# Kernel optimization log

Measured on AMD Instinct MI355X. Metric: run time of the kernel, lower is better.

## Reference

```python
import jax, jax.numpy as jnp
import numpy as np

N = 4096
NFEAT = 512
NHID = 64
NHEADS = 8
NCLASS = 41
ALPHA = 0.2          # LeakyReLU negative slope
NEG = -9e15          # mask fill value from the torch code
EDGE_P = 0.004       # ~16 avg degree


def _xavier_uniform(key, shape, gain=1.414):
    fan_in, fan_out = shape[-2], shape[-1]
    limit = gain * np.sqrt(6.0 / (fan_in + fan_out))
    return jax.random.uniform(key, shape, jnp.float32, -limit, limit)


def setup_inputs() -> dict:
    key = jax.random.key(0)
    ks = jax.random.split(key, 6)
    x = jax.random.normal(ks[0], (N, NFEAT), jnp.float32)
    # sparse random graph, densified (module calls adj.to_dense()); add self-loops
    adj = (jax.random.uniform(ks[1], (N, N)) < EDGE_P).astype(jnp.float32)
    adj = jnp.maximum(adj, jnp.eye(N, dtype=jnp.float32))
    # 8 attention heads (nfeat -> nhid), stacked
    W_heads = _xavier_uniform(ks[2], (NHEADS, NFEAT, NHID))
    a_heads = _xavier_uniform(ks[3], (NHEADS, 2 * NHID, 1))
    # output attention layer (nhid*nheads -> nclass)
    W_out = _xavier_uniform(ks[4], (NHEADS * NHID, NCLASS))
    a_out = _xavier_uniform(ks[5], (2 * NCLASS, 1))
    return {"x": x, "adj": adj, "W_heads": W_heads, "a_heads": a_heads,
            "W_out": W_out, "a_out": a_out}


def _leaky_relu(e):
    return jnp.where(e > 0, e, ALPHA * e)


def reference(x, adj, W_heads, a_heads, W_out, a_out):
    # inference mode: all dropout layers are identity (training=False)
    mask = adj > 0                                   # [N, N]
    # ---- multi-head GAT layer (concat=True, ELU inside layer) ----
    Wh = jnp.einsum('nf,hfd->hnd', x, W_heads)       # [H, N, D]
    a1 = a_heads[:, :NHID, 0]                        # [H, D]
    a2 = a_heads[:, NHID:, 0]                        # [H, D]
    s1 = jnp.einsum('hnd,hd->hn', Wh, a1)            # [H, N]
    s2 = jnp.einsum('hnd,hd->hn', Wh, a2)            # [H, N]
    e = _leaky_relu(s1[:, :, None] + s2[:, None, :])  # [H, N, N]
    att = jax.nn.softmax(jnp.where(mask[None], e, NEG), axis=-1)
    h = jax.nn.elu(jnp.einsum('hnm,hmd->hnd', att, Wh))   # [H, N, D]
    h = jnp.transpose(h, (1, 0, 2)).reshape(N, NHEADS * NHID)  # concat heads
    # ---- output GAT layer (concat=False) + ELU (with_relu=True) ----
    Wh2 = h @ W_out                                  # [N, C]
    e2 = _leaky_relu(Wh2 @ a_out[:NCLASS] + (Wh2 @ a_out[NCLASS:]).T)  # [N, N]
    att2 = jax.nn.softmax(jnp.where(mask, e2, NEG), axis=-1)
    out = jax.nn.elu(att2 @ Wh2)                     # [N, C]
    # mode='t', multi_label falsy -> log_softmax
    return jax.nn.log_softmax(out, axis=1)
```

## Files before the change

### kernel.cpp

```cpp
#include <hip/hip_runtime.h>
#include <hip/hip_bf16.h>
#include <math.h>


#define N 4096
#define NFEAT 512
#define NHID 64
#define NHEADS 8
#define NCLASS 41
#define NCPAD 48
#define ALPHA 0.2f
#define ELLW 64

using short8  = __attribute__((ext_vector_type(8))) short;
using floatx4 = __attribute__((ext_vector_type(4))) float;

__device__ __forceinline__ float wred_max(float v) {
#pragma unroll
  for (int o = 32; o; o >>= 1) v = fmaxf(v, __shfl_xor(v, o, 64));
  return v;
}
__device__ __forceinline__ float wred_sum(float v) {
#pragma unroll
  for (int o = 32; o; o >>= 1) v += __shfl_xor(v, o, 64);
  return v;
}

__device__ __forceinline__ void split_bf16(float v, short& hi, short& lo) {
  __hip_bfloat16 hb = __float2bfloat16(v);
  float hf = __bfloat162float(hb);
  __hip_bfloat16 lb = __float2bfloat16(v - hf);
  hi = *reinterpret_cast<short*>(&hb);
  lo = *reinterpret_cast<short*>(&lb);
}

__global__ __launch_bounds__(256) void setup(const float* __restrict__ x,
                                             const float* __restrict__ W,
                                             const float* __restrict__ W_out,
                                             const float* __restrict__ adj,
                                             short* __restrict__ Xhi,
                                             short* __restrict__ Xlo,
                                             short* __restrict__ Wthi,
                                             short* __restrict__ Wtlo,
                                             short* __restrict__ WOhi,
                                             short* __restrict__ WOlo,
                                             int* __restrict__ cols,
                                             int* __restrict__ cnts) {
  if (blockIdx.x < 4096) {
    __shared__ int c;
    const int row = blockIdx.x;
    if (threadIdx.x == 0) c = 0;
    __syncthreads();
    const float4* arow = (const float4*)(adj + (size_t)row * N);
    for (int j4 = threadIdx.x; j4 < N / 4; j4 += 256) {
      float4 v = arow[j4];
      if (v.x > 0.f) { int p = atomicAdd(&c, 1); if (p < ELLW) cols[row * ELLW + p] = j4 * 4 + 0; }
      if (v.y > 0.f) { int p = atomicAdd(&c, 1); if (p < ELLW) cols[row * ELLW + p] = j4 * 4 + 1; }
      if (v.z > 0.f) { int p = atomicAdd(&c, 1); if (p < ELLW) cols[row * ELLW + p] = j4 * 4 + 2; }
      if (v.w > 0.f) { int p = atomicAdd(&c, 1); if (p < ELLW) cols[row * ELLW + p] = j4 * 4 + 3; }
    }
    __syncthreads();
    if (threadIdx.x == 0) cnts[row] = min(c, ELLW);
  } else if (blockIdx.x < 6144) {
    const int t = (blockIdx.x - 4096) * 256 + threadIdx.x;
    const float4 v = ((const float4*)x)[t];
    short h0, l0, h1, l1, h2, l2, h3, l3;
    split_bf16(v.x, h0, l0);
    split_bf16(v.y, h1, l1);
    split_bf16(v.z, h2, l2);
    split_bf16(v.w, h3, l3);
    ((short4*)Xhi)[t] = make_short4(h0, h1, h2, h3);
    ((short4*)Xlo)[t] = make_short4(l0, l1, l2, l3);
  } else if (blockIdx.x < 6208) {
    __shared__ float tile[64][65];
    const int idx = blockIdx.x - 6144;
    const int h = idx >> 3, k0 = (idx & 7) * 64;
    const int t = threadIdx.x;
#pragma unroll
    for (int i = 0; i < 4; i++) {
      const int g = t + 256 * i;
      const int r = g >> 4, c4 = g & 15;
      const float4 v = *(const float4*)&W[(size_t)h * 32768 + (size_t)(k0 + r) * 64 + c4 * 4];
      tile[r][c4 * 4 + 0] = v.x;
      tile[r][c4 * 4 + 1] = v.y;
      tile[r][c4 * 4 + 2] = v.z;
      tile[r][c4 * 4 + 3] = v.w;
    }
    __syncthreads();
#pragma unroll
    for (int i = 0; i < 2; i++) {
      const int g = t + 256 * i;
      const int d = g >> 3, kg = (g & 7) * 8;
      short8 hv, lv;
#pragma unroll
      for (int j = 0; j < 8; j++) {
        short hh, ll;
        split_bf16(tile[kg + j][d], hh, ll);
        hv[j] = hh;
        lv[j] = ll;
      }
      const size_t dst = (size_t)h * 32768 + (size_t)d * 512 + k0 + kg;
      *(short8*)&Wthi[dst] = hv;
      *(short8*)&Wtlo[dst] = lv;
    }
  } else {
    const int t = (blockIdx.x - 6208) * 256 + threadIdx.x;
    const int c = t >> 9, k = t & 511;
    float v = (c < NCLASS) ? W_out[(size_t)k * NCLASS + c] : 0.f;
    short hi, lo;
    split_bf16(v, hi, lo);
    WOhi[c * 512 + k] = hi;
    WOlo[c * 512 + k] = lo;
  }
}

__global__ __launch_bounds__(128) void wh_gemm_mfma(
    const short* __restrict__ Xhi, const short* __restrict__ Xlo,
    const short* __restrict__ Wthi, const short* __restrict__ Wtlo,
    const float* __restrict__ a_heads,
    float* __restrict__ Wh, float* __restrict__ s1, float* __restrict__ s2) {
  __shared__ __align__(16) short Ahi[64 * 72];
  __shared__ __align__(16) short Alo[64 * 72];
  __shared__ __align__(16) short Bhi[64 * 72];
  __shared__ __align__(16) short Blo[64 * 72];
  const int id = blockIdx.x;
  const int h = (id >> 3) & 7;
  const int tile = (id & 7) + ((id >> 6) << 3);
  const int n0 = tile * 64;
  const int tid = threadIdx.x;
  const int w = tid >> 6, L = tid & 63;

  floatx4 acc[2][4];
#pragma unroll
  for (int rt = 0; rt < 2; rt++)
#pragma unroll
    for (int f = 0; f < 4; f++) acc[rt][f] = (floatx4){0.f, 0.f, 0.f, 0.f};

  for (int k0 = 0; k0 < NFEAT; k0 += 64) {
    __syncthreads();
#pragma unroll
    for (int i = 0; i < 4; i++) {
      const int g = tid + 128 * i;
      const int row = g >> 3, kg = (g & 7) * 8;
      const size_t asrc = (size_t)(n0 + row) * NFEAT + k0 + kg;
      *(uint4*)&Ahi[row * 72 + kg] = *(const uint4*)&Xhi[asrc];
      *(uint4*)&Alo[row * 72 + kg] = *(const uint4*)&Xlo[asrc];
      const size_t bsrc = (size_t)h * 32768 + (size_t)row * 512 + k0 + kg;
      *(uint4*)&Bhi[row * 72 + kg] = *(const uint4*)&Wthi[bsrc];
      *(uint4*)&Blo[row * 72 + kg] = *(const uint4*)&Wtlo[bsrc];
    }
    __syncthreads();
#pragma unroll
    for (int ks = 0; ks < 2; ks++) {
      const int koff = ks * 32 + (L >> 4) * 8;
      const int abase = (w * 32 + (L & 15)) * 72 + koff;
      short8 ahi0 = *(const short8*)&Ahi[abase];
      short8 alo0 = *(const short8*)&Alo[abase];
      short8 ahi1 = *(const short8*)&Ahi[abase + 16 * 72];
      short8 alo1 = *(const short8*)&Alo[abase + 16 * 72];
#pragma unroll
      for (int f = 0; f < 4; f++) {
        short8 bhi = *(const short8*)&Bhi[(f * 16 + (L & 15)) * 72 + koff];
        short8 blo = *(const short8*)&Blo[(f * 16 + (L & 15)) * 72 + koff];
        acc[0][f] = __builtin_amdgcn_mfma_f32_16x16x32_bf16(ahi0, bhi, acc[0][f], 0, 0, 0);
        acc[0][f] = __builtin_amdgcn_mfma_f32_16x16x32_bf16(ahi0, blo, acc[0][f], 0, 0, 0);
        acc[0][f] = __builtin_amdgcn_mfma_f32_16x16x32_bf16(alo0, bhi, acc[0][f], 0, 0, 0);
        acc[1][f] = __builtin_amdgcn_mfma_f32_16x16x32_bf16(ahi1, bhi, acc[1][f], 0, 0, 0);
        acc[1][f] = __builtin_amdgcn_mfma_f32_16x16x32_bf16(ahi1, blo, acc[1][f], 0, 0, 0);
        acc[1][f] = __builtin_amdgcn_mfma_f32_16x16x32_bf16(alo1, bhi, acc[1][f], 0, 0, 0);
      }
    }
  }

  const int q = L >> 4, c16 = L & 15;
  float a1v[4], a2v[4];
#pragma unroll
  for (int f = 0; f < 4; f++) {
    a1v[f] = a_heads[h * 128 + f * 16 + c16];
    a2v[f] = a_heads[h * 128 + 64 + f * 16 + c16];
  }
#pragma unroll
  for (int rt = 0; rt < 2; rt++) {
    float p1[4] = {0.f, 0.f, 0.f, 0.f}, p2[4] = {0.f, 0.f, 0.f, 0.f};
#pragma unroll
    for (int f = 0; f < 4; f++)
#pragma unroll
      for (int r = 0; r < 4; r++) {
        const float vv = acc[rt][f][r];
        const int row = n0 + w * 32 + rt * 16 + q * 4 + r;
        Wh[((size_t)(h << 12) + row) * NHID + f * 16 + c16] = vv;
        p1[r] += vv * a1v[f];
        p2[r] += vv * a2v[f];
      }
#pragma unroll
    for (int r = 0; r < 4; r++)
#pragma unroll
      for (int o = 1; o < 16; o <<= 1) {
        p1[r] += __shfl_xor(p1[r], o, 64);
        p2[r] += __shfl_xor(p2[r], o, 64);
      }
    if (c16 == 0) {
      const int row = n0 + w * 32 + rt * 16 + q * 4;
#pragma unroll
      for (int r = 0; r < 4; r++) {
        s1[(h << 12) + row + r] = p1[r];
        s2[(h << 12) + row + r] = p2[r];
      }
    }
  }
}

__global__ __launch_bounds__(256) void att1_kernel(
    const float* __restrict__ Wh, const float* __restrict__ s1,
    const float* __restrict__ s2, const int* __restrict__ cols,
    const int* __restrict__ cnts, short* __restrict__ Hhi,
    short* __restrict__ Hlo) {
  __shared__ float pj[4][64];
  __shared__ int jj[4][64];
  const int w = threadIdx.x >> 6, lane = threadIdx.x & 63;
  const int pair = blockIdx.x * 4 + w;
  const int h = pair >> 12, i = pair & (N - 1);
  const int cnt = cnts[i];
  const float s1i = s1[(h << 12) + i];
  const float* s2h = s2 + (h << 12);
  float e0 = -1e30f;
  int j0 = 0;
  if (lane < cnt) {
    j0 = cols[i * ELLW + lane];
    float t = s1i + s2h[j0];
    e0 = t > 0.f ? t : ALPHA * t;
  }
  const float m = wred_max(e0);
  float p = (lane < cnt) ? expf(e0 - m) : 0.f;
  const float S = wred_sum(p);
  p *= 1.f / S;
  pj[w][lane] = p;
  jj[w][lane] = (lane < cnt) ? j0 : 0;
  __syncthreads();
  const int grp = lane >> 3, c8 = lane & 7;
  const float* Whh = Wh + (((size_t)h << 12)) * NHID;
  float4 a0 = make_float4(0.f, 0.f, 0.f, 0.f);
  float4 a1 = make_float4(0.f, 0.f, 0.f, 0.f);
  for (int t0 = 0; t0 < cnt; t0 += 8) {
    const float pt = pj[w][t0 + grp];
    const int jt = jj[w][t0 + grp];
    const float4 v0 = *(const float4*)&Whh[(size_t)jt * NHID + c8 * 8];
    const float4 v1 = *(const float4*)&Whh[(size_t)jt * NHID + c8 * 8 + 4];
    a0.x += pt * v0.x; a0.y += pt * v0.y; a0.z += pt * v0.z; a0.w += pt * v0.w;
    a1.x += pt * v1.x; a1.y += pt * v1.y; a1.z += pt * v1.z; a1.w += pt * v1.w;
  }
#pragma unroll
  for (int off = 8; off <= 32; off <<= 1) {
    a0.x += __shfl_xor(a0.x, off, 64);
    a0.y += __shfl_xor(a0.y, off, 64);
    a0.z += __shfl_xor(a0.z, off, 64);
    a0.w += __shfl_xor(a0.w, off, 64);
    a1.x += __shfl_xor(a1.x, off, 64);
    a1.y += __shfl_xor(a1.y, off, 64);
    a1.z += __shfl_xor(a1.z, off, 64);
    a1.w += __shfl_xor(a1.w, off, 64);
  }
  if (grp == 0) {
    float o[8] = {a0.x, a0.y, a0.z, a0.w, a1.x, a1.y, a1.z, a1.w};
    short8 hv, lv;
#pragma unroll
    for (int j = 0; j < 8; j++) {
      const float e = o[j] > 0.f ? o[j] : expf(o[j]) - 1.f;
      short hh, ll;
      split_bf16(e, hh, ll);
      hv[j] = hh;
      lv[j] = ll;
    }
    const size_t base = (size_t)i * 512 + h * 64 + c8 * 8;
    *(short8*)&Hhi[base] = hv;
    *(short8*)&Hlo[base] = lv;
  }
}

__global__ __launch_bounds__(256) void gemm2_mfma(
    const short* __restrict__ Hhi, const short* __restrict__ Hlo,
    const short* __restrict__ WOhi, const short* __restrict__ WOlo,
    const float* __restrict__ a_out,
    float* __restrict__ Wh2, float* __restrict__ s1b, float* __restrict__ s2b) {
  __shared__ float red[3][64][12];
  const int n0 = blockIdx.x * 16;
  const int tid = threadIdx.x;
  const int w = tid >> 6, L = tid & 63;
  const int r15 = L & 15;

  floatx4 acc[3];
#pragma unroll
  for (int f = 0; f < 3; f++) acc[f] = (floatx4){0.f, 0.f, 0.f, 0.f};

#pragma unroll
  for (int ks = 0; ks < 4; ks++) {
    const int koff = w * 128 + ks * 32 + (L >> 4) * 8;
    const short8 ahi = *(const short8*)&Hhi[(size_t)(n0 + r15) * 512 + koff];
    const short8 alo = *(const short8*)&Hlo[(size_t)(n0 + r15) * 512 + koff];
#pragma unroll
    for (int f = 0; f < 3; f++) {
      const short8 bhi = *(const short8*)&WOhi[(size_t)(f * 16 + r15) * 512 + koff];
      const short8 blo = *(const short8*)&WOlo[(size_t)(f * 16 + r15) * 512 + koff];
      acc[f] = __builtin_amdgcn_mfma_f32_16x16x32_bf16(ahi, bhi, acc[f], 0, 0, 0);
      acc[f] = __builtin_amdgcn_mfma_f32_16x16x32_bf16(ahi, blo, acc[f], 0, 0, 0);
      acc[f] = __builtin_amdgcn_mfma_f32_16x16x32_bf16(alo, bhi, acc[f], 0, 0, 0);
    }
  }

  if (w) {
#pragma unroll
    for (int f = 0; f < 3; f++)
#pragma unroll
      for (int r = 0; r < 4; r++) red[w - 1][L][f * 4 + r] = acc[f][r];
  }
  __syncthreads();
  if (w == 0) {
    const int q = L >> 4, c16 = r15;
    float a1v[3], a2v[3];
#pragma unroll
    for (int f = 0; f < 3; f++) {
      const int col = f * 16 + c16;
      a1v[f] = (col < NCLASS) ? a_out[col] : 0.f;
      a2v[f] = (col < NCLASS) ? a_out[NCLASS + col] : 0.f;
    }
    float p1[4] = {0.f, 0.f, 0.f, 0.f}, p2[4] = {0.f, 0.f, 0.f, 0.f};
#pragma unroll
    for (int f = 0; f < 3; f++)
#pragma unroll
      for (int r = 0; r < 4; r++) {
        const float vv = acc[f][r] + red[0][L][f * 4 + r] + red[1][L][f * 4 + r] +
                         red[2][L][f * 4 + r];
        const int col = f * 16 + c16;
        const int row = n0 + q * 4 + r;
        if (col < NCLASS) Wh2[(size_t)row * NCLASS + col] = vv;
        p1[r] += vv * a1v[f];
        p2[r] += vv * a2v[f];
      }
#pragma unroll
    for (int r = 0; r < 4; r++)
#pragma unroll
      for (int o = 1; o < 16; o <<= 1) {
        p1[r] += __shfl_xor(p1[r], o, 64);
        p2[r] += __shfl_xor(p2[r], o, 64);
      }
    if (c16 == 0) {
      const int row = n0 + q * 4;
#pragma unroll
      for (int r = 0; r < 4; r++) {
        s1b[row + r] = p1[r];
        s2b[row + r] = p2[r];
      }
    }
  }
}

__global__ __launch_bounds__(256) void att2_kernel(const float* __restrict__ Wh2,
                                                   const float* __restrict__ s1b,
                                                   const float* __restrict__ s2b,
                                                   const int* __restrict__ cols,
                                                   const int* __restrict__ cnts,
                                                   float* __restrict__ out) {
  __shared__ float pj[4][64];
  __shared__ int jj[4][64];
  const int w = threadIdx.x >> 6, lane = threadIdx.x & 63;
  const int i = blockIdx.x * 4 + w;
  const int cnt = cnts[i];
  const float s1i = s1b[i];
  float e0 = -1e30f;
  int j0 = 0;
  if (lane < cnt) {
    j0 = cols[i * ELLW + lane];
    float t = s1i + s2b[j0];
    e0 = t > 0.f ? t : ALPHA * t;
  }
  const float m = wred_max(e0);
  float p = (lane < cnt) ? expf(e0 - m) : 0.f;
  const float S = wred_sum(p);
  p *= 1.f / S;
  pj[w][lane] = p;
  jj[w][lane] = (lane < cnt) ? j0 : 0;
  __syncthreads();
  float acc = 0.f;
  for (int t = 0; t < cnt; t++) {
    const float pt = pj[w][t];
    const int jt = jj[w][t];
    if (lane < NCLASS) acc += pt * Wh2[(size_t)jt * NCLASS + lane];
  }
  const float o = acc > 0.f ? acc : expf(acc) - 1.f;
  const float vv = (lane < NCLASS) ? o : -1e30f;
  const float mm = wred_max(vv);
  const float ex = (lane < NCLASS) ? expf(o - mm) : 0.f;
  const float SS = wred_sum(ex);
  if (lane < NCLASS) out[(size_t)i * NCLASS + lane] = o - mm - logf(SS);
}

extern "C" void kernel_launch(void* const* d_in, const int* in_sizes, int n_in,
                              void* d_out, int out_size, void* d_ws, size_t ws_size,
                              hipStream_t stream) {
  const float* x       = (const float*)d_in[0];
  const float* adj     = (const float*)d_in[1];
  const float* W_heads = (const float*)d_in[2];
  const float* a_heads = (const float*)d_in[3];
  const float* W_out   = (const float*)d_in[4];
  const float* a_out   = (const float*)d_in[5];
  float* out = (float*)d_out;

  float* ws   = (float*)d_ws;
  float* Wh   = ws;
  float* s1   = Wh + (size_t)NHEADS * N * NHID;
  float* s2   = s1 + NHEADS * N;
  float* Wh2  = s2 + NHEADS * N;
  float* s1b  = Wh2 + (size_t)N * NCLASS;
  float* s2b  = s1b + N;
  int* cnts   = (int*)(s2b + N);
  int* cols   = cnts + N;
  short* Xhi  = (short*)(cols + N * ELLW);
  short* Xlo  = Xhi + (size_t)N * NFEAT;
  short* Wthi = Xlo + (size_t)N * NFEAT;
  short* Wtlo = Wthi + (size_t)NHEADS * NHID * NFEAT;
  short* WOhi = Wtlo + (size_t)NHEADS * NHID * NFEAT;
  short* WOlo = WOhi + (size_t)NCPAD * 512;
  short* Hhi  = WOlo + (size_t)NCPAD * 512;
  short* Hlo  = Hhi + (size_t)N * NFEAT;

  hipLaunchKernelGGL(setup, dim3(6304), dim3(256), 0, stream,
                     x, W_heads, W_out, adj, Xhi, Xlo, Wthi, Wtlo, WOhi, WOlo, cols, cnts);
  hipLaunchKernelGGL(wh_gemm_mfma, dim3(NHEADS * N / 64), dim3(128), 0, stream,
                     Xhi, Xlo, Wthi, Wtlo, a_heads, Wh, s1, s2);
  hipLaunchKernelGGL(att1_kernel, dim3(NHEADS * N / 4), dim3(256), 0, stream,
                     Wh, s1, s2, cols, cnts, Hhi, Hlo);
  hipLaunchKernelGGL(gemm2_mfma, dim3(N / 16), dim3(256), 0, stream,
                     Hhi, Hlo, WOhi, WOlo, a_out, Wh2, s1b, s2b);
  hipLaunchKernelGGL(att2_kernel, dim3(N / 4), dim3(256), 0, stream,
                     Wh2, s1b, s2b, cols, cnts, out);
}
```

Before: 160.1 us.

## Drop LDS staging in Wh GEMM, load MFMA operands directly from global

Rewrites the per-head Wh GEMM so each wave loads its bf16 hi/lo A and B fragments straight from global memory instead of staging 64x64 tiles in shared memory with barriers. Blocks grow to 4 waves, each owning a 16-row slice, which removes the __syncthreads and LDS traffic. The cost is that B fragments are no longer shared through LDS, so each wave re-reads them from global/L2 and gets less reuse per load.

```diff
diff --git a/kernel.cpp b/kernel.cpp
--- a/kernel.cpp
+++ b/kernel.cpp
@@ -114,98 +114,73 @@
   }
 }
 
-__global__ __launch_bounds__(128) void wh_gemm_mfma(
+__global__ __launch_bounds__(256) void wh_gemm_mfma(
     const short* __restrict__ Xhi, const short* __restrict__ Xlo,
     const short* __restrict__ Wthi, const short* __restrict__ Wtlo,
     const float* __restrict__ a_heads,
     float* __restrict__ Wh, float* __restrict__ s1, float* __restrict__ s2) {
-  __shared__ __align__(16) short Ahi[64 * 72];
-  __shared__ __align__(16) short Alo[64 * 72];
-  __shared__ __align__(16) short Bhi[64 * 72];
-  __shared__ __align__(16) short Blo[64 * 72];
   const int id = blockIdx.x;
   const int h = (id >> 3) & 7;
   const int tile = (id & 7) + ((id >> 6) << 3);
   const int n0 = tile * 64;
-  const int tid = threadIdx.x;
-  const int w = tid >> 6, L = tid & 63;
-
-  floatx4 acc[2][4];
-#pragma unroll
-  for (int rt = 0; rt < 2; rt++)
-#pragma unroll
-    for (int f = 0; f < 4; f++) acc[rt][f] = (floatx4){0.f, 0.f, 0.f, 0.f};
-
-  for (int k0 = 0; k0 < NFEAT; k0 += 64) {
-    __syncthreads();
-#pragma unroll
-    for (int i = 0; i < 4; i++) {
-      const int g = tid + 128 * i;
-      const int row = g >> 3, kg = (g & 7) * 8;
-      const size_t asrc = (size_t)(n0 + row) * NFEAT + k0 + kg;
-      *(uint4*)&Ahi[row * 72 + kg] = *(const uint4*)&Xhi[asrc];
-      *(uint4*)&Alo[row * 72 + kg] = *(const uint4*)&Xlo[asrc];
-      const size_t bsrc = (size_t)h * 32768 + (size_t)row * 512 + k0 + kg;
-      *(uint4*)&Bhi[row * 72 + kg] = *(const uint4*)&Wthi[bsrc];
-      *(uint4*)&Blo[row * 72 + kg] = *(const uint4*)&Wtlo[bsrc];
-    }
-    __syncthreads();
-#pragma unroll
-    for (int ks = 0; ks < 2; ks++) {
-      const int koff = ks * 32 + (L >> 4) * 8;
-      const int abase = (w * 32 + (L & 15)) * 72 + koff;
-      short8 ahi0 = *(const short8*)&Ahi[abase];
-      short8 alo0 = *(const short8*)&Alo[abase];
-      short8 ahi1 = *(const short8*)&Ahi[abase + 16 * 72];
-      short8 alo1 = *(const short8*)&Alo[abase + 16 * 72];
-#pragma unroll
-      for (int f = 0; f < 4; f++) {
-        short8 bhi = *(const short8*)&Bhi[(f * 16 + (L & 15)) * 72 + koff];
-        short8 blo = *(const short8*)&Blo[(f * 16 + (L & 15)) * 72 + koff];
-        acc[0][f] = __builtin_amdgcn_mfma_f32_16x16x32_bf16(ahi0, bhi, acc[0][f], 0, 0, 0);
-        acc[0][f] = __builtin_amdgcn_mfma_f32_16x16x32_bf16(ahi0, blo, acc[0][f], 0, 0, 0);
-        acc[0][f] = __builtin_amdgcn_mfma_f32_16x16x32_bf16(alo0, bhi, acc[0][f], 0, 0, 0);
-        acc[1][f] = __builtin_amdgcn_mfma_f32_16x16x32_bf16(ahi1, bhi, acc[1][f], 0, 0, 0);
-        acc[1][f] = __builtin_amdgcn_mfma_f32_16x16x32_bf16(ahi1, blo, acc[1][f], 0, 0, 0);
-        acc[1][f] = __builtin_amdgcn_mfma_f32_16x16x32_bf16(alo1, bhi, acc[1][f], 0, 0, 0);
-      }
-    }
-  }
-
-  const int q = L >> 4, c16 = L & 15;
+  const int w = threadIdx.x >> 6, L = threadIdx.x & 63;
+  const int q = L >> 4, r15 = L & 15;
+
+  floatx4 acc[4];
+#pragma unroll
+  for (int f = 0; f < 4; f++) acc[f] = (floatx4){0.f, 0.f, 0.f, 0.f};
+
+  const short* Ah = Xhi + (size_t)(n0 + w * 16 + r15) * NFEAT;
+  const short* Al = Xlo + (size_t)(n0 + w * 16 + r15) * NFEAT;
+  const short* Bh = Wthi + (size_t)h * 32768 + (size_t)r15 * 512;
+  const short* Bl = Wtlo + (size_t)h * 32768 + (size_t)r15 * 512;
+
+#pragma unroll 2
+  for (int ks = 0; ks < 16; ks++) {
+    const int ko = ks * 32 + q * 8;
+    const short8 ahi = *(const short8*)&Ah[ko];
+    const short8 alo = *(const short8*)&Al[ko];
+#pragma unroll
+    for (int f = 0; f < 4; f++) {
+      const short8 bhi = *(const short8*)&Bh[f * 16 * 512 + ko];
+      const short8 blo = *(const short8*)&Bl[f * 16 * 512 + ko];
+      acc[f] = __builtin_amdgcn_mfma_f32_16x16x32_bf16(ahi, bhi, acc[f], 0, 0, 0);
+      acc[f] = __builtin_amdgcn_mfma_f32_16x16x32_bf16(ahi, blo, acc[f], 0, 0, 0);
+      acc[f] = __builtin_amdgcn_mfma_f32_16x16x32_bf16(alo, bhi, acc[f], 0, 0, 0);
+    }
+  }
+
+  const int c16 = r15;
   float a1v[4], a2v[4];
 #pragma unroll
   for (int f = 0; f < 4; f++) {
     a1v[f] = a_heads[h * 128 + f * 16 + c16];
     a2v[f] = a_heads[h * 128 + 64 + f * 16 + c16];
   }
-#pragma unroll
-  for (int rt = 0; rt < 2; rt++) {
-    float p1[4] = {0.f, 0.f, 0.f, 0.f}, p2[4] = {0.f, 0.f, 0.f, 0.f};
-#pragma unroll
-    for (int f = 0; f < 4; f++)
-#pragma unroll
-      for (int r = 0; r < 4; r++) {
-        const float vv = acc[rt][f][r];
-        const int row = n0 + w * 32 + rt * 16 + q * 4 + r;
-        Wh[((size_t)(h << 12) + row) * NHID + f * 16 + c16] = vv;
-        p1[r] += vv * a1v[f];
-        p2[r] += vv * a2v[f];
-      }
-#pragma unroll
-    for (int r = 0; r < 4; r++)
-#pragma unroll
-      for (int o = 1; o < 16; o <<= 1) {
-        p1[r] += __shfl_xor(p1[r], o, 64);
-        p2[r] += __shfl_xor(p2[r], o, 64);
-      }
-    if (c16 == 0) {
-      const int row = n0 + w * 32 + rt * 16 + q * 4;
-#pragma unroll
-      for (int r = 0; r < 4; r++) {
-        s1[(h << 12) + row + r] = p1[r];
-        s2[(h << 12) + row + r] = p2[r];
-      }
+  float p1[4] = {0.f, 0.f, 0.f, 0.f}, p2[4] = {0.f, 0.f, 0.f, 0.f};
+#pragma unroll
+  for (int f = 0; f < 4; f++)
+#pragma unroll
+    for (int r = 0; r < 4; r++) {
+      const float vv = acc[f][r];
+      const int row = n0 + w * 16 + q * 4 + r;
+      Wh[((size_t)(h << 12) + row) * NHID + f * 16 + c16] = vv;
+      p1[r] += vv * a1v[f];
+      p2[r] += vv * a2v[f];
+    }
+#pragma unroll
+  for (int r = 0; r < 4; r++)
+#pragma unroll
+    for (int o = 1; o < 16; o <<= 1) {
+      p1[r] += __shfl_xor(p1[r], o, 64);
+      p2[r] += __shfl_xor(p2[r], o, 64);
+    }
+  if (c16 == 0) {
+    const int row = n0 + w * 16 + q * 4;
+#pragma unroll
+    for (int r = 0; r < 4; r++) {
+      s1[(h << 12) + row + r] = p1[r];
+      s2[(h << 12) + row + r] = p2[r];
     }
   }
 }
@@ -425,7 +400,7 @@
 
   hipLaunchKernelGGL(setup, dim3(6304), dim3(256), 0, stream,
                      x, W_heads, W_out, adj, Xhi, Xlo, Wthi, Wtlo, WOhi, WOlo, cols, cnts);
-  hipLaunchKernelGGL(wh_gemm_mfma, dim3(NHEADS * N / 64), dim3(128), 0, stream,
+  hipLaunchKernelGGL(wh_gemm_mfma, dim3(NHEADS * N / 64), dim3(256), 0, stream,
                      Xhi, Xlo, Wthi, Wtlo, a_heads, Wh, s1, s2);
   hipLaunchKernelGGL(att1_kernel, dim3(NHEADS * N / 4), dim3(256), 0, stream,
                      Wh, s1, s2, cols, cnts, Hhi, Hlo);
```

Measured after the change: 184.8 us. 1.15x slower.

## Double-buffer LDS tiles with register prefetch in Wh GEMM

Applied to the files above, without the earlier changes.

The Wh projection GEMM now prefetches the next K-tile of X and W (hi/lo bf16 splits) into registers while MFMAs run on the current LDS buffer, then writes them to the alternate LDS buffer. This removes one barrier per iteration and overlaps global loads with compute. In exchange it doubles shared memory to about 73KB per block and adds 16 uint4 registers per thread, which may lower occupancy. This GEMM is only one of several kernels in the GAT pipeline, so its effect on total time is bounded.

```diff
diff --git a/kernel.cpp b/kernel.cpp
--- a/kernel.cpp
+++ b/kernel.cpp
@@ -119,10 +119,10 @@
     const short* __restrict__ Wthi, const short* __restrict__ Wtlo,
     const float* __restrict__ a_heads,
     float* __restrict__ Wh, float* __restrict__ s1, float* __restrict__ s2) {
-  __shared__ __align__(16) short Ahi[64 * 72];
-  __shared__ __align__(16) short Alo[64 * 72];
-  __shared__ __align__(16) short Bhi[64 * 72];
-  __shared__ __align__(16) short Blo[64 * 72];
+  __shared__ __align__(16) short Ahi[2][64 * 72];
+  __shared__ __align__(16) short Alo[2][64 * 72];
+  __shared__ __align__(16) short Bhi[2][64 * 72];
+  __shared__ __align__(16) short Blo[2][64 * 72];
   const int id = blockIdx.x;
   const int h = (id >> 3) & 7;
   const int tile = (id & 7) + ((id >> 6) << 3);
@@ -136,32 +136,53 @@
 #pragma unroll
     for (int f = 0; f < 4; f++) acc[rt][f] = (floatx4){0.f, 0.f, 0.f, 0.f};
 
-  for (int k0 = 0; k0 < NFEAT; k0 += 64) {
-    __syncthreads();
-#pragma unroll
-    for (int i = 0; i < 4; i++) {
-      const int g = tid + 128 * i;
-      const int row = g >> 3, kg = (g & 7) * 8;
-      const size_t asrc = (size_t)(n0 + row) * NFEAT + k0 + kg;
-      *(uint4*)&Ahi[row * 72 + kg] = *(const uint4*)&Xhi[asrc];
-      *(uint4*)&Alo[row * 72 + kg] = *(const uint4*)&Xlo[asrc];
-      const size_t bsrc = (size_t)h * 32768 + (size_t)row * 512 + k0 + kg;
-      *(uint4*)&Bhi[row * 72 + kg] = *(const uint4*)&Wthi[bsrc];
-      *(uint4*)&Blo[row * 72 + kg] = *(const uint4*)&Wtlo[bsrc];
-    }
-    __syncthreads();
+  uint4 rAhi[4], rAlo[4], rBhi[4], rBlo[4];
+
+#define STAGE_LOAD(K0)                                                       \
+  {                                                                          \
+    _Pragma("unroll") for (int i = 0; i < 4; i++) {                          \
+      const int g = tid + 128 * i;                                           \
+      const int row = g >> 3, kg = (g & 7) * 8;                              \
+      const size_t asrc = (size_t)(n0 + row) * NFEAT + (K0) + kg;            \
+      rAhi[i] = *(const uint4*)&Xhi[asrc];                                   \
+      rAlo[i] = *(const uint4*)&Xlo[asrc];                                   \
+      const size_t bsrc = (size_t)h * 32768 + (size_t)row * 512 + (K0) + kg; \
+      rBhi[i] = *(const uint4*)&Wthi[bsrc];                                  \
+      rBlo[i] = *(const uint4*)&Wtlo[bsrc];                                  \
+    }                                                                        \
+  }
+
+#define STAGE_WRITE(BUF)                                                     \
+  {                                                                          \
+    _Pragma("unroll") for (int i = 0; i < 4; i++) {                          \
+      const int g = tid + 128 * i;                                           \
+      const int row = g >> 3, kg = (g & 7) * 8;                              \
+      *(uint4*)&Ahi[BUF][row * 72 + kg] = rAhi[i];                           \
+      *(uint4*)&Alo[BUF][row * 72 + kg] = rAlo[i];                           \
+      *(uint4*)&Bhi[BUF][row * 72 + kg] = rBhi[i];                           \
+      *(uint4*)&Blo[BUF][row * 72 + kg] = rBlo[i];                           \
+    }                                                                        \
+  }
+
+  STAGE_LOAD(0);
+  STAGE_WRITE(0);
+  __syncthreads();
+
+  int cur = 0;
+  for (int kt = 0; kt < 8; kt++) {
+    if (kt < 7) STAGE_LOAD((kt + 1) * 64);
 #pragma unroll
     for (int ks = 0; ks < 2; ks++) {
       const int koff = ks * 32 + (L >> 4) * 8;
       const int abase = (w * 32 + (L & 15)) * 72 + koff;
-      short8 ahi0 = *(const short8*)&Ahi[abase];
-      short8 alo0 = *(const short8*)&Alo[abase];
-      short8 ahi1 = *(const short8*)&Ahi[abase + 16 * 72];
-      short8 alo1 = *(const short8*)&Alo[abase + 16 * 72];
+      short8 ahi0 = *(const short8*)&Ahi[cur][abase];
+      short8 alo0 = *(const short8*)&Alo[cur][abase];
+      short8 ahi1 = *(const short8*)&Ahi[cur][abase + 16 * 72];
+      short8 alo1 = *(const short8*)&Alo[cur][abase + 16 * 72];
 #pragma unroll
       for (int f = 0; f < 4; f++) {
-        short8 bhi = *(const short8*)&Bhi[(f * 16 + (L & 15)) * 72 + koff];
-        short8 blo = *(const short8*)&Blo[(f * 16 + (L & 15)) * 72 + koff];
+        short8 bhi = *(const short8*)&Bhi[cur][(f * 16 + (L & 15)) * 72 + koff];
+        short8 blo = *(const short8*)&Blo[cur][(f * 16 + (L & 15)) * 72 + koff];
         acc[0][f] = __builtin_amdgcn_mfma_f32_16x16x32_bf16(ahi0, bhi, acc[0][f], 0, 0, 0);
         acc[0][f] = __builtin_amdgcn_mfma_f32_16x16x32_bf16(ahi0, blo, acc[0][f], 0, 0, 0);
         acc[0][f] = __builtin_amdgcn_mfma_f32_16x16x32_bf16(alo0, bhi, acc[0][f], 0, 0, 0);
@@ -170,7 +191,14 @@
         acc[1][f] = __builtin_amdgcn_mfma_f32_16x16x32_bf16(alo1, bhi, acc[1][f], 0, 0, 0);
       }
     }
-  }
+    if (kt < 7) {
+      STAGE_WRITE(cur ^ 1);
+      __syncthreads();
+    }
+    cur ^= 1;
+  }
+#undef STAGE_LOAD
+#undef STAGE_WRITE
 
   const int q = L >> 4, c16 = L & 15;
   float a1v[4], a2v[4];
```

New measurement: 159.3 us, median of 2. Within noise of the previous version (-0.5%).
